# Kernel tuning notes

Measured on AMD Instinct MI355X. Metric: run time of the kernel, lower is better.

The kernel has to match this reference:

```python
import jax, jax.numpy as jnp
import numpy as np

B, T, E, H, D, NL = 2, 1024, 2048, 16, 128, 3
MAXL = T * (2 ** (NL - 1))  # k length doubles each layer: T, 2T, 4T


def _rms_norm(x, w, eps=1e-5):
    return x * jax.lax.rsqrt(jnp.mean(x * x, axis=-1, keepdims=True) + eps) * w


def _rope(x, cos, sin):
    # x: [B, S, H, D]; cos/sin: [>=S, D/2]; GPT-NeoX style (non-interleaved)
    S = x.shape[1]
    c = cos[:S][None, :, None, :]
    s = sin[:S][None, :, None, :]
    x1, x2 = jnp.split(x, 2, axis=-1)
    return jnp.concatenate([x1 * c - x2 * s, x1 * s + x2 * c], axis=-1)


def _causal_attn(q, k, v):
    # bottom-right-aligned causal (flash_attn_func causal=True with kv longer than q)
    Tq, L = q.shape[1], k.shape[1]
    scale = 1.0 / np.sqrt(q.shape[-1]).astype(np.float32)
    scores = jnp.einsum('bthd,bshd->bhts', q, k) * scale
    i = jnp.arange(Tq)[:, None]
    j = jnp.arange(L)[None, :]
    mask = j <= i + (L - Tq)
    scores = jnp.where(mask[None, None], scores, -jnp.inf)
    p = jax.nn.softmax(scores, axis=-1)
    return jnp.einsum('bhts,bshd->bthd', p, v)


def setup_inputs() -> dict:
    key = jax.random.key(0)
    ks = jax.random.split(key, 6)
    x = jax.random.normal(ks[0], (B, T, E), dtype=jnp.float32)
    inv_freq = 1.0 / (10000.0 ** (np.arange(0, D, 2, dtype=np.float32) / D))  # [D/2]
    ang = np.arange(MAXL, dtype=np.float32)[:, None] * inv_freq[None, :]      # [MAXL, D/2]
    cos = jnp.asarray(np.cos(ang), dtype=jnp.float32)
    sin = jnp.asarray(np.sin(ang), dtype=jnp.float32)
    wq = jax.random.normal(ks[1], (NL, E, E), dtype=jnp.float32) * 0.02
    wk = jax.random.normal(ks[2], (NL, E, E), dtype=jnp.float32) * 0.02
    wv = jax.random.normal(ks[3], (NL, E, E), dtype=jnp.float32) * 0.02
    ln_w = jnp.ones((NL, E), dtype=jnp.float32)
    lambdas = jnp.zeros((NL,), dtype=jnp.float32)
    w_out = jax.random.normal(ks[4], (E, E), dtype=jnp.float32) * 0.02
    final_ln_w = jnp.ones((E,), dtype=jnp.float32)
    alpha = jnp.ones((1,), dtype=jnp.float32)
    return {'x': x, 'cos': cos, 'sin': sin, 'wq': wq, 'wk': wk, 'wv': wv,
            'ln_w': ln_w, 'lambdas': lambdas, 'w_out': w_out,
            'final_ln_w': final_ln_w, 'alpha': alpha}


def reference(x, cos, sin, wq, wk, wv, ln_w, lambdas, w_out, final_ln_w, alpha):
    bsz, tgt_len, embed_dim = x.shape
    # lambda weights: sigmoid then LayerNorm over the NL scalars (no affine)
    lam = jax.nn.sigmoid(lambdas)
    lam = (lam - jnp.mean(lam)) * jax.lax.rsqrt(jnp.var(lam) + 1e-5)
    acc_k, acc_v = [], []
    total = jnp.zeros_like(x)
    for i in range(NL):  # small fixed layer count
        q = (x @ wq[i].T).reshape(bsz, tgt_len, H, D)
        k = (x @ wk[i].T).reshape(bsz, tgt_len, H, D)
        v = (x @ wv[i].T).reshape(bsz, tgt_len, H, D)
        if i > 0:
            k = jnp.concatenate([k] + acc_k, axis=1)
            v = jnp.concatenate([v] + acc_v, axis=1)
        q = _rope(q, cos, sin)
        k = _rope(k, cos, sin)  # note: cached K gets rotary re-applied, as in source
        attn = _causal_attn(q, k, v).reshape(bsz, tgt_len, embed_dim)
        attn = _rms_norm(attn, ln_w[i])
        total = total + attn * lam[i]
        acc_k.append(k)
        acc_v.append(v)
    out = _rms_norm(total + alpha * x, final_ln_w)
    return out @ w_out.T
```

## Files before the change

kernel.cpp:

```cpp
#include <hip/hip_runtime.h>
#include <hip/hip_bf16.h>

typedef unsigned short ushort_t;
typedef __attribute__((ext_vector_type(8))) short bf16x8;
typedef __attribute__((ext_vector_type(4))) short bf16x4;
typedef __attribute__((ext_vector_type(4))) float f32x4;
typedef __attribute__((ext_vector_type(4))) unsigned short u16x4;
typedef __attribute__((ext_vector_type(4))) unsigned int u32x4;

#define DEV __device__ __forceinline__

DEV ushort_t f2bf(float f) {
  __hip_bfloat16 h = __float2bfloat16(f);
  return __builtin_bit_cast(unsigned short, h);
}
DEV float bf2f(ushort_t b) {
  union { float f; unsigned int u; } a; a.u = ((unsigned int)b) << 16;
  return a.f;
}
DEV void gload_lds16(const void* g, void* l) {
  __builtin_amdgcn_global_load_lds((const __attribute__((address_space(1))) void*)g,
                                   (__attribute__((address_space(3))) void*)l, 16, 0, 0);
}
DEV unsigned ldsaddr(const void* l) {
  return (unsigned)(unsigned long long)(const __attribute__((address_space(3))) void*)l;
}
template <int OFF>
DEV bf16x4 tr16o(unsigned a) {
  bf16x4 d;
  asm volatile("ds_read_b64_tr_b16 %0, %1 offset:%c2" : "=v"(d) : "v"(a), "i"(OFF));
  return d;
}
template <int OFF>
DEV bf16x8 ldsb128o(unsigned a) {
  bf16x8 d;
  asm volatile("ds_read_b128 %0, %1 offset:%c2" : "=v"(d) : "v"(a), "i"(OFF));
  return d;
}

__global__ __launch_bounds__(256) void f2b_kernel(const float* __restrict__ in,
                                                  ushort_t* __restrict__ out, int n) {
  int base = (blockIdx.x * 256 + threadIdx.x) * 4;
  if (base >= n) return;
  f32x4 v = *(const f32x4*)(in + base);
  u16x4 o;
  o.x = f2bf(v.x); o.y = f2bf(v.y); o.z = f2bf(v.z); o.w = f2bf(v.w);
  *(u16x4*)(out + base) = o;
}

__global__ __launch_bounds__(256) void f2b3_kernel(const float* __restrict__ a, const float* __restrict__ b,
                                                   const float* __restrict__ c, ushort_t* __restrict__ out) {
  int id = blockIdx.x * 256 + threadIdx.x;
  int sel = id >> 20, k = (id & 1048575) * 4;
  const float* src = sel == 0 ? a : sel == 1 ? b : c;
  f32x4 v = *(const f32x4*)(src + k);
  u16x4 o;
  o.x = f2bf(v.x); o.y = f2bf(v.y); o.z = f2bf(v.z); o.w = f2bf(v.w);
  *(u16x4*)(out + (size_t)sel * 4194304 + k) = o;
}

__global__ void lam_kernel(const float* __restrict__ lambdas, float* __restrict__ lam) {
  if (threadIdx.x == 0 && blockIdx.x == 0) {
    float l0 = 1.f / (1.f + __expf(-lambdas[0]));
    float l1 = 1.f / (1.f + __expf(-lambdas[1]));
    float l2 = 1.f / (1.f + __expf(-lambdas[2]));
    float mean = (l0 + l1 + l2) * (1.f / 3.f);
    float d0 = l0 - mean, d1 = l1 - mean, d2 = l2 - mean;
    float var = (d0 * d0 + d1 * d1 + d2 * d2) * (1.f / 3.f);
    float rs = rsqrtf(var + 1e-5f);
    lam[0] = d0 * rs; lam[1] = d1 * rs; lam[2] = d2 * rs;
  }
}

DEV void gemm_core(const ushort_t* __restrict__ A, const ushort_t* __restrict__ Bm,
                   ushort_t* lsA, ushort_t* lsB, int bm, int bn, int kbeg, int kend,
                   f32x4 (&acc)[4][4]) {
  const int K = 2048;
  int tid = threadIdx.x;
  int w = tid >> 6, lane = tid & 63;
  int g = lane >> 4, r = lane & 15;
  int wm = w >> 1, wn = w & 1;
#pragma unroll
  for (int i = 0; i < 4; ++i)
#pragma unroll
    for (int j = 0; j < 4; ++j) acc[i][j] = 0.f;

  for (int kk = kbeg; kk < kend; kk += 32) {
    __syncthreads();
#pragma unroll
    for (int j2 = 0; j2 < 2; ++j2) {
      int eb = w * 1024 + j2 * 512;
      int ebl = eb + lane * 8;
      int rr = ebl >> 5, cc = ebl & 31;
      gload_lds16(A + (size_t)(bm * 128 + rr) * K + kk + cc, lsA + eb);
      gload_lds16(Bm + (size_t)(bn * 128 + rr) * K + kk + cc, lsB + eb);
    }
    __syncthreads();
    bf16x8 af[4], bfr[4];
#pragma unroll
    for (int i = 0; i < 4; ++i)
      af[i] = *(const bf16x8*)(lsA + (wm * 64 + i * 16 + r) * 32 + g * 8);
#pragma unroll
    for (int j = 0; j < 4; ++j)
      bfr[j] = *(const bf16x8*)(lsB + (wn * 64 + j * 16 + r) * 32 + g * 8);
#pragma unroll
    for (int i = 0; i < 4; ++i)
#pragma unroll
      for (int j = 0; j < 4; ++j)
        acc[i][j] = __builtin_amdgcn_mfma_f32_16x16x32_bf16(af[i], bfr[j], acc[i][j], 0, 0, 0);
  }
}

__global__ __launch_bounds__(256) void gemm_qkv(
    const ushort_t* __restrict__ A,
    const ushort_t* __restrict__ Bq, const ushort_t* __restrict__ Bk, const ushort_t* __restrict__ Bv,
    ushort_t* __restrict__ Cq, ushort_t* __restrict__ Ck, ushort_t* __restrict__ Cv, int Lkv) {
  __shared__ __align__(16) ushort_t lsA[4096];
  __shared__ __align__(16) ushort_t lsB[4096];
  int sel = blockIdx.x >> 4, bn = blockIdx.x & 15, bm = blockIdx.y;
  const ushort_t* Bm = (sel == 0) ? Bq : (sel == 1) ? Bk : Bv;
  ushort_t* C = (sel == 0) ? Cq : (sel == 1) ? Ck : Cv;
  int Lsel = (sel == 0) ? 1024 : Lkv;
  f32x4 acc[4][4];
  gemm_core(A, Bm, lsA, lsB, bm, bn, 0, 2048, acc);
  int lane = threadIdx.x & 63, w = threadIdx.x >> 6;
  int g = lane >> 4, r = lane & 15, wm = w >> 1, wn = w & 1;
#pragma unroll
  for (int i = 0; i < 4; ++i)
#pragma unroll
    for (int j = 0; j < 4; ++j) {
      int row0 = bm * 128 + wm * 64 + i * 16 + g * 4;
      int col = bn * 128 + wn * 64 + j * 16 + r;
#pragma unroll
      for (int t = 0; t < 4; ++t) {
        int row = row0 + t;
        int b2 = row >> 10, t2 = row & 1023;
        C[(size_t)(b2 * Lsel + t2) * 2048 + col] = f2bf(acc[i][j][t]);
      }
    }
}

__global__ __launch_bounds__(256) void gemm_bt_part(
    const ushort_t* __restrict__ A, const ushort_t* __restrict__ Bm, float* __restrict__ P) {
  __shared__ __align__(16) ushort_t lsA[4096];
  __shared__ __align__(16) ushort_t lsB[4096];
  int bn = blockIdx.x, bm = blockIdx.y, s = blockIdx.z;
  f32x4 acc[4][4];
  gemm_core(A, Bm, lsA, lsB, bm, bn, s * 1024, (s + 1) * 1024, acc);
  float* C = P + (size_t)s * 4194304;
  int lane = threadIdx.x & 63, w = threadIdx.x >> 6;
  int g = lane >> 4, r = lane & 15, wm = w >> 1, wn = w & 1;
#pragma unroll
  for (int i = 0; i < 4; ++i)
#pragma unroll
    for (int j = 0; j < 4; ++j) {
      int row0 = bm * 128 + wm * 64 + i * 16 + g * 4;
      int col = bn * 128 + wn * 64 + j * 16 + r;
#pragma unroll
      for (int t = 0; t < 4; ++t)
        C[(size_t)(row0 + t) * 2048 + col] = acc[i][j][t];
    }
}

__global__ __launch_bounds__(256) void add2_kernel(const float* __restrict__ a, const float* __restrict__ b,
                                                   float* __restrict__ out) {
  int i = (blockIdx.x * 256 + threadIdx.x) * 4;
  f32x4 va = *(const f32x4*)(a + i);
  f32x4 vb = *(const f32x4*)(b + i);
  f32x4 r;
#pragma unroll
  for (int k = 0; k < 4; ++k) r[k] = va[k] + vb[k];
  *(f32x4*)(out + i) = r;
}

DEV void rope_body(const ushort_t* src, ushort_t* dst, const float* cosT, const float* sinT,
                   int Ls, int s0, int Ld, int dpos0, int cnt, int bp) {
  int b = bp / cnt, pidx = bp % cnt;
  int pos = dpos0 + pidx;
  int pi = threadIdx.x * 4;
  int h = pi >> 6, d = pi & 63;
  const ushort_t* s_ = src + ((size_t)(b * Ls + s0 + pidx) * 16 + h) * 128 + d;
  ushort_t* d_ = dst + ((size_t)(b * Ld + pos) * 16 + h) * 128 + d;
  f32x4 c4 = *(const f32x4*)(cosT + (size_t)pos * 64 + d);
  f32x4 s4 = *(const f32x4*)(sinT + (size_t)pos * 64 + d);
  u16x4 x1 = *(const u16x4*)(s_);
  u16x4 x2 = *(const u16x4*)(s_ + 64);
  u16x4 o1, o2;
#pragma unroll
  for (int k = 0; k < 4; ++k) {
    float a = bf2f(x1[k]), bb = bf2f(x2[k]);
    o1[k] = f2bf(a * c4[k] - bb * s4[k]);
    o2[k] = f2bf(a * s4[k] + bb * c4[k]);
  }
  *(u16x4*)d_ = o1;
  *(u16x4*)(d_ + 64) = o2;
}
DEV void copy_body(const ushort_t* src, ushort_t* dst, int Ls, int s0, int Ld, int dpos0,
                   int cnt, int bp) {
  int b = bp / cnt, pidx = bp % cnt;
  const u32x4* s = (const u32x4*)(src + (size_t)(b * Ls + s0 + pidx) * 2048);
  u32x4* d = (u32x4*)(dst + (size_t)(b * Ld + dpos0 + pidx) * 2048);
  d[threadIdx.x] = s[threadIdx.x];
}

__global__ __launch_bounds__(256) void rope_k(ushort_t* Kc, const float* __restrict__ cosT,
                                              const float* __restrict__ sinT, int L) {
  rope_body(Kc, Kc, cosT, sinT, L, 0, L, 0, 1024, blockIdx.x);
}

__global__ __launch_bounds__(256) void layer1_cache(const ushort_t* __restrict__ K0, ushort_t* __restrict__ K1,
                                                    const ushort_t* __restrict__ V0, ushort_t* __restrict__ V1,
                                                    const float* __restrict__ cosT, const float* __restrict__ sinT) {
  int bp = blockIdx.x;
  if (bp < 2048) rope_body(K0, K1, cosT, sinT, 1024, 0, 2048, 1024, 1024, bp);
  else copy_body(V0, V1, 1024, 0, 2048, 1024, 1024, bp - 2048);
}

__global__ __launch_bounds__(256) void layer2_cache(const ushort_t* __restrict__ K1, ushort_t* __restrict__ K2,
                                                    const ushort_t* __restrict__ V1, ushort_t* __restrict__ V2,
                                                    const float* __restrict__ cosT, const float* __restrict__ sinT) {
  int bp = blockIdx.x;
  if (bp < 2048) copy_body(K1, K2, 2048, 1024, 4096, 1024, 1024, bp);
  else if (bp < 6144) rope_body(K1, K2, cosT, sinT, 2048, 0, 4096, 2048, 2048, bp - 2048);
  else if (bp < 8192) copy_body(V1, V2, 2048, 1024, 4096, 1024, 1024, bp - 6144);
  else copy_body(V1, V2, 2048, 0, 4096, 2048, 2048, bp - 8192);
}

__global__ __launch_bounds__(256, 4) void attn_kernel(
    const ushort_t* __restrict__ Qraw, const ushort_t* __restrict__ Kc, const ushort_t* __restrict__ Vc,
    const float* __restrict__ cosT, const float* __restrict__ sinT,
    ushort_t* __restrict__ Opart, float2* __restrict__ Ml, int Lk) {
  __shared__ __align__(16) ushort_t lsK[8192];
  __shared__ __align__(16) ushort_t lsV[8192];
  const float SC2 = 0.1275174366f;

  int bid = (int)blockIdx.x;
  int swz = (bid & 7) * 128 + (bid >> 3);
  int s = swz & 1;
  int rest = swz >> 1;

  int w = threadIdx.x >> 6, lane = threadIdx.x & 63;
  int bq = rest & 15, h = (rest >> 4) & 15, b = rest >> 8;
  int qt = bq * 4 + w;
  int g = lane >> 4, r = lane & 15;
  int off = Lk - 1024;

  const ushort_t* qbase = Qraw + ((size_t)(b * 1024 + qt * 16 + r) * 16 + h) * 128;
  int pos = qt * 16 + r;
  const float* cb = cosT + (size_t)pos * 64;
  const float* sb = sinT + (size_t)pos * 64;
  bf16x8 qf[4];
#pragma unroll
  for (int c = 0; c < 2; ++c) {
    int d0 = c * 32 + g * 8;
    f32x4 c0 = *(const f32x4*)(cb + d0);
    f32x4 c1 = *(const f32x4*)(cb + d0 + 4);
    f32x4 s0 = *(const f32x4*)(sb + d0);
    f32x4 s1 = *(const f32x4*)(sb + d0 + 4);
    bf16x8 x1 = *(const bf16x8*)(qbase + d0);
    bf16x8 x2 = *(const bf16x8*)(qbase + d0 + 64);
    bf16x8 lo, hi;
#pragma unroll
    for (int k = 0; k < 8; ++k) {
      float cv = (k < 4 ? c0[k] : c1[k - 4]) * SC2;
      float sv = (k < 4 ? s0[k] : s1[k - 4]) * SC2;
      float a = bf2f((ushort_t)x1[k]);
      float bb = bf2f((ushort_t)x2[k]);
      lo[k] = (short)f2bf(a * cv - bb * sv);
      hi[k] = (short)f2bf(a * sv + bb * cv);
    }
    qf[c] = lo; qf[c + 2] = hi;
  }

  int t = threadIdx.x;
  int krow0 = t >> 4,        kc0 = (t & 15) ^ (krow0 & 7);
  int krow1 = (t + 256) >> 4, kc1 = (t & 15) ^ (krow1 & 7);
  const size_t adv = 32 * 2048;
  const size_t adv2 = 2 * adv;
  const ushort_t* srcK0 = Kc + ((size_t)(b * Lk + krow0) * 16 + h) * 128 + kc0 * 8 + s * adv;
  const ushort_t* srcK1 = Kc + ((size_t)(b * Lk + krow1) * 16 + h) * 128 + kc1 * 8 + s * adv;
  int L0 = t, L1 = t + 256;
  int vrow0 = ((L0 >> 3) & 7) * 4 + ((L0 >> 1) & 3), vd0 = (L0 >> 6) * 16 + (L0 & 1) * 8;
  int vrow1 = ((L1 >> 3) & 7) * 4 + ((L1 >> 1) & 3), vd1 = (L1 >> 6) * 16 + (L1 & 1) * 8;
  const ushort_t* srcV0 = Vc + ((size_t)(b * Lk + vrow0) * 16 + h) * 128 + vd0 + s * adv;
  const ushort_t* srcV1 = Vc + ((size_t)(b * Lk + vrow1) * 16 + h) * 128 + vd1 + s * adv;

  auto STAGE = [&](int buf) {
    ushort_t* k0 = lsK + buf * 4096 + w * 512;
    ushort_t* v0 = lsV + buf * 4096 + w * 512;
    gload_lds16(srcK0, k0);
    gload_lds16(srcK1, k0 + 2048);
    gload_lds16(srcV0, v0);
    gload_lds16(srcV1, v0 + 2048);
    srcK0 += adv2; srcK1 += adv2; srcV0 += adv2; srcV1 += adv2;
  };

  unsigned kx[4];
  unsigned kbase0 = ldsaddr(lsK) + (unsigned)(r * 256);
#pragma unroll
  for (int c = 0; c < 4; ++c)
    kx[c] = kbase0 + (unsigned)((((c * 32 + g * 8) ^ ((r & 7) * 8))) * 2);
  unsigned vbase0 = ldsaddr(lsV);

  float m_run = -1e30f, l_run = 0.f;
  f32x4 o[8];
#pragma unroll
  for (int c = 0; c < 8; ++c) o[c] = 0.f;

  int qp = qt * 16 + r + off;
  int qmin = qt * 16 + off;
  int nkt_w = ((qt * 16 + 15 + off) >> 5) + 1;
  int nkt_blk = (((bq * 4 + 3) * 16 + 15 + off) >> 5) + 1;
  int ntile = (nkt_blk - s + 1) >> 1;

#define LDK(c, ks) ldsb128o<(ks) * 4096>(kx[c] + kb)
#define LDV(hh, i) tr16o<(hh) * 4096 + (i) * 512>(vb)

  if (ntile > 0) {
    STAGE(0);
    for (int it = 0; it < ntile; ++it) {
      int kt = s + it * 2;
      int cur = it & 1;
      if (it + 1 < ntile) {
        STAGE(cur ^ 1);
        asm volatile("s_waitcnt vmcnt(4)" ::: "memory");
      } else {
        asm volatile("s_waitcnt vmcnt(0)" ::: "memory");
      }
      __builtin_amdgcn_s_barrier();
      __builtin_amdgcn_sched_barrier(0);
      if (kt < nkt_w) {
        unsigned kb = (unsigned)(cur << 13);
        unsigned vb = vbase0 + kb;
        f32x4 st[2];
        {
          bf16x8 k0 = LDK(0, 0), k1 = LDK(1, 0), k2 = LDK(2, 0), k3 = LDK(3, 0);
          asm volatile("s_waitcnt lgkmcnt(0)" ::: "memory");
          __builtin_amdgcn_sched_barrier(0);
          __builtin_amdgcn_s_setprio(1);
          f32x4 acc = 0.f;
          acc = __builtin_amdgcn_mfma_f32_16x16x32_bf16(k0, qf[0], acc, 0, 0, 0);
          acc = __builtin_amdgcn_mfma_f32_16x16x32_bf16(k1, qf[1], acc, 0, 0, 0);
          acc = __builtin_amdgcn_mfma_f32_16x16x32_bf16(k2, qf[2], acc, 0, 0, 0);
          acc = __builtin_amdgcn_mfma_f32_16x16x32_bf16(k3, qf[3], acc, 0, 0, 0);
          __builtin_amdgcn_s_setprio(0);
          st[0] = acc;
        }
        {
          bf16x8 k0 = LDK(0, 1), k1 = LDK(1, 1), k2 = LDK(2, 1), k3 = LDK(3, 1);
          asm volatile("s_waitcnt lgkmcnt(0)" ::: "memory");
          __builtin_amdgcn_sched_barrier(0);
          __builtin_amdgcn_s_setprio(1);
          f32x4 acc = 0.f;
          acc = __builtin_amdgcn_mfma_f32_16x16x32_bf16(k0, qf[0], acc, 0, 0, 0);
          acc = __builtin_amdgcn_mfma_f32_16x16x32_bf16(k1, qf[1], acc, 0, 0, 0);
          acc = __builtin_amdgcn_mfma_f32_16x16x32_bf16(k2, qf[2], acc, 0, 0, 0);
          acc = __builtin_amdgcn_mfma_f32_16x16x32_bf16(k3, qf[3], acc, 0, 0, 0);
          __builtin_amdgcn_s_setprio(0);
          st[1] = acc;
        }
        float pmax = -1e30f;
        int kp0 = kt * 32;
        if (kp0 + 31 > qmin) {
#pragma unroll
          for (int ks = 0; ks < 2; ++ks)
#pragma unroll
            for (int j = 0; j < 4; ++j) {
              int key = kp0 + ks * 16 + g * 4 + j;
              float sv = st[ks][j];
              if (key > qp) sv = -1e30f;
              st[ks][j] = sv;
              pmax = fmaxf(pmax, sv);
            }
        } else {
#pragma unroll
          for (int ks = 0; ks < 2; ++ks)
#pragma unroll
            for (int j = 0; j < 4; ++j) pmax = fmaxf(pmax, st[ks][j]);
        }
        pmax = fmaxf(pmax, __shfl_xor(pmax, 16, 64));
        pmax = fmaxf(pmax, __shfl_xor(pmax, 32, 64));
        if (!__all(pmax <= m_run + 11.5f)) {
          float mnew = fmaxf(m_run, pmax);
          float corr = exp2f(m_run - mnew);
          l_run *= corr;
#pragma unroll
          for (int c = 0; c < 8; ++c)
#pragma unroll
            for (int tt = 0; tt < 4; ++tt) o[c][tt] *= corr;
          m_run = mnew;
        }
        float psum = 0.f;
        bf16x4 pf[2];
#pragma unroll
        for (int ks = 0; ks < 2; ++ks)
#pragma unroll
          for (int j = 0; j < 4; ++j) {
            float pe = exp2f(st[ks][j] - m_run);
            psum += pe;
            pf[ks][j] = (short)f2bf(pe);
          }
        psum += __shfl_xor(psum, 16, 64);
        psum += __shfl_xor(psum, 32, 64);
        l_run += psum;
        {
          bf16x4 v0 = LDV(0, 0), v1 = LDV(0, 1), v2 = LDV(0, 2), v3 = LDV(0, 3);
          bf16x4 v4 = LDV(0, 4), v5 = LDV(0, 5), v6 = LDV(0, 6), v7 = LDV(0, 7);
          asm volatile("s_waitcnt lgkmcnt(0)" ::: "memory");
          __builtin_amdgcn_sched_barrier(0);
          __builtin_amdgcn_s_setprio(1);
          o[0] = __builtin_amdgcn_mfma_f32_16x16x16bf16_1k(v0, pf[0], o[0], 0, 0, 0);
          o[0] = __builtin_amdgcn_mfma_f32_16x16x16bf16_1k(v1, pf[1], o[0], 0, 0, 0);
          o[1] = __builtin_amdgcn_mfma_f32_16x16x16bf16_1k(v2, pf[0], o[1], 0, 0, 0);
          o[1] = __builtin_amdgcn_mfma_f32_16x16x16bf16_1k(v3, pf[1], o[1], 0, 0, 0);
          o[2] = __builtin_amdgcn_mfma_f32_16x16x16bf16_1k(v4, pf[0], o[2], 0, 0, 0);
          o[2] = __builtin_amdgcn_mfma_f32_16x16x16bf16_1k(v5, pf[1], o[2], 0, 0, 0);
          o[3] = __builtin_amdgcn_mfma_f32_16x16x16bf16_1k(v6, pf[0], o[3], 0, 0, 0);
          o[3] = __builtin_amdgcn_mfma_f32_16x16x16bf16_1k(v7, pf[1], o[3], 0, 0, 0);
          __builtin_amdgcn_s_setprio(0);
        }
        {
          bf16x4 v0 = LDV(1, 0), v1 = LDV(1, 1), v2 = LDV(1, 2), v3 = LDV(1, 3);
          bf16x4 v4 = LDV(1, 4), v5 = LDV(1, 5), v6 = LDV(1, 6), v7 = LDV(1, 7);
          asm volatile("s_waitcnt lgkmcnt(0)" ::: "memory");
          __builtin_amdgcn_sched_barrier(0);
          __builtin_amdgcn_s_setprio(1);
          o[4] = __builtin_amdgcn_mfma_f32_16x16x16bf16_1k(v0, pf[0], o[4], 0, 0, 0);
          o[4] = __builtin_amdgcn_mfma_f32_16x16x16bf16_1k(v1, pf[1], o[4], 0, 0, 0);
          o[5] = __builtin_amdgcn_mfma_f32_16x16x16bf16_1k(v2, pf[0], o[5], 0, 0, 0);
          o[5] = __builtin_amdgcn_mfma_f32_16x16x16bf16_1k(v3, pf[1], o[5], 0, 0, 0);
          o[6] = __builtin_amdgcn_mfma_f32_16x16x16bf16_1k(v4, pf[0], o[6], 0, 0, 0);
          o[6] = __builtin_amdgcn_mfma_f32_16x16x16bf16_1k(v5, pf[1], o[6], 0, 0, 0);
          o[7] = __builtin_amdgcn_mfma_f32_16x16x16bf16_1k(v6, pf[0], o[7], 0, 0, 0);
          o[7] = __builtin_amdgcn_mfma_f32_16x16x16bf16_1k(v7, pf[1], o[7], 0, 0, 0);
          __builtin_amdgcn_s_setprio(0);
        }
      }
      __builtin_amdgcn_sched_barrier(0);
      __builtin_amdgcn_s_barrier();
    }
  }
#undef LDK
#undef LDV
  ushort_t* ob = Opart + (size_t)s * 4194304 + ((size_t)(b * 1024 + qt * 16 + r) * 16 + h) * 128;
#pragma unroll
  for (int dblk = 0; dblk < 8; ++dblk) {
    u16x4 ov;
#pragma unroll
    for (int tt = 0; tt < 4; ++tt) ov[tt] = f2bf(o[dblk][tt]);
    *(u16x4*)(ob + dblk * 16 + g * 4) = ov;
  }
  if (g == 0) {
    float2 ml; ml.x = m_run; ml.y = l_run;
    Ml[((size_t)(s * 2 + b) * 1024 + qt * 16 + r) * 16 + h] = ml;
  }
}

template <int FIRST>
__global__ __launch_bounds__(256) void rms_combine(const ushort_t* __restrict__ Opart, const float2* __restrict__ Ml,
                                                   const float* __restrict__ lnw, const float* __restrict__ lam,
                                                   int li, float* __restrict__ total) {
  int row = blockIdx.x;
  int t8 = threadIdx.x * 8;
  int h = t8 >> 7;
  float2 ml0 = Ml[(size_t)row * 16 + h];
  float2 ml1 = Ml[(size_t)(row + 2048) * 16 + h];
  float M = fmaxf(ml0.x, ml1.x);
  float w0 = exp2f(ml0.x - M), w1 = exp2f(ml1.x - M);
  float rinv = 1.f / (w0 * ml0.y + w1 * ml1.y);
  w0 *= rinv; w1 *= rinv;
  const ushort_t* a0 = Opart + (size_t)row * 2048 + t8;
  const ushort_t* a1 = a0 + 4194304;
  u16x4 p00 = *(const u16x4*)(a0);
  u16x4 p01 = *(const u16x4*)(a0 + 4);
  u16x4 p10 = *(const u16x4*)(a1);
  u16x4 p11 = *(const u16x4*)(a1 + 4);
  f32x4 v0, v1;
#pragma unroll
  for (int k = 0; k < 4; ++k) {
    v0[k] = w0 * bf2f(p00[k]) + w1 * bf2f(p10[k]);
    v1[k] = w0 * bf2f(p01[k]) + w1 * bf2f(p11[k]);
  }
  float ss = v0.x * v0.x + v0.y * v0.y + v0.z * v0.z + v0.w * v0.w +
             v1.x * v1.x + v1.y * v1.y + v1.z * v1.z + v1.w * v1.w;
#pragma unroll
  for (int m = 1; m < 64; m <<= 1) ss += __shfl_xor(ss, m, 64);
  __shared__ float red[4];
  int w = threadIdx.x >> 6, lane = threadIdx.x & 63;
  if (lane == 0) red[w] = ss;
  __syncthreads();
  ss = red[0] + red[1] + red[2] + red[3];
  float sca = rsqrtf(ss * (1.f / 2048.f) + 1e-5f) * lam[li];
  f32x4 w0v = *(const f32x4*)(lnw + t8);
  f32x4 w1v = *(const f32x4*)(lnw + t8 + 4);
  float* o = total + (size_t)row * 2048 + t8;
  f32x4 r0, r1;
#pragma unroll
  for (int k = 0; k < 4; ++k) { r0[k] = v0[k] * sca * w0v[k]; r1[k] = v1[k] * sca * w1v[k]; }
  if (!FIRST) {
    f32x4 q0 = *(const f32x4*)(o);
    f32x4 q1 = *(const f32x4*)(o + 4);
#pragma unroll
    for (int k = 0; k < 4; ++k) { r0[k] += q0[k]; r1[k] += q1[k]; }
  }
  *(f32x4*)(o) = r0;
  *(f32x4*)(o + 4) = r1;
}

__global__ __launch_bounds__(256) void final_norm(const float* __restrict__ total, const float* __restrict__ x,
                                                  const float* __restrict__ alphap, const float* __restrict__ flw,
                                                  ushort_t* __restrict__ ybf) {
  int row = blockIdx.x;
  float al = alphap[0];
  int t8 = threadIdx.x * 8;
  const float* tp = total + (size_t)row * 2048 + t8;
  const float* xp = x + (size_t)row * 2048 + t8;
  f32x4 t0 = *(const f32x4*)(tp);
  f32x4 t1 = *(const f32x4*)(tp + 4);
  f32x4 x0 = *(const f32x4*)(xp);
  f32x4 x1 = *(const f32x4*)(xp + 4);
  float y[8];
#pragma unroll
  for (int k = 0; k < 4; ++k) { y[k] = t0[k] + al * x0[k]; y[4 + k] = t1[k] + al * x1[k]; }
  float ss = 0.f;
#pragma unroll
  for (int k = 0; k < 8; ++k) ss += y[k] * y[k];
#pragma unroll
  for (int m = 1; m < 64; m <<= 1) ss += __shfl_xor(ss, m, 64);
  __shared__ float red[4];
  int w = threadIdx.x >> 6, lane = threadIdx.x & 63;
  if (lane == 0) red[w] = ss;
  __syncthreads();
  ss = red[0] + red[1] + red[2] + red[3];
  float s = rsqrtf(ss * (1.f / 2048.f) + 1e-5f);
  f32x4 w0 = *(const f32x4*)(flw + t8);
  f32x4 w1 = *(const f32x4*)(flw + t8 + 4);
  u16x4 o0, o1;
#pragma unroll
  for (int k = 0; k < 4; ++k) {
    o0[k] = f2bf(y[k] * s * w0[k]);
    o1[k] = f2bf(y[4 + k] * s * w1[k]);
  }
  *(u16x4*)(ybf + (size_t)row * 2048 + t8) = o0;
  *(u16x4*)(ybf + (size_t)row * 2048 + t8 + 4) = o1;
}

extern "C" void kernel_launch(void* const* d_in, const int* in_sizes, int n_in,
                              void* d_out, int out_size, void* d_ws, size_t ws_size,
                              hipStream_t stream) {
  const float* x = (const float*)d_in[0];
  const float* cosT = (const float*)d_in[1];
  const float* sinT = (const float*)d_in[2];
  const float* wq = (const float*)d_in[3];
  const float* wk = (const float*)d_in[4];
  const float* wv = (const float*)d_in[5];
  const float* lnw = (const float*)d_in[6];
  const float* lambdas = (const float*)d_in[7];
  const float* w_out = (const float*)d_in[8];
  const float* flw = (const float*)d_in[9];
  const float* alpha = (const float*)d_in[10];

  const size_t ME = 4194304ull;
  char* p = (char*)d_ws;
  size_t off = 0;
  auto alc = [&](size_t bytes) -> void* {
    void* r = p + off;
    off += (bytes + 255) & ~(size_t)255;
    return r;
  };
  ushort_t* xb = (ushort_t*)alc(ME * 2);
  void* uni = alc(2 * ME * 4);
  ushort_t* wl = (ushort_t*)uni;
  ushort_t* Opart = (ushort_t*)uni;
  float* Ppart = (float*)uni;
  ushort_t* q = (ushort_t*)alc(ME * 2);
  ushort_t* K0 = (ushort_t*)alc(ME * 2);
  ushort_t* K1 = (ushort_t*)alc(2 * ME * 2);
  ushort_t* K2 = (ushort_t*)alc(4 * ME * 2);
  ushort_t* V0 = (ushort_t*)alc(ME * 2);
  ushort_t* V1 = (ushort_t*)alc(2 * ME * 2);
  ushort_t* V2 = (ushort_t*)alc(4 * ME * 2);
  float* total = (float*)alc(ME * 4);
  float2* Ml = (float2*)alc(65536 * 8);
  float* lam = (float*)alc(256);
  ushort_t* ybf = q;
  ushort_t* wob = K0;

  f2b_kernel<<<4096, 256, 0, stream>>>(x, xb, 4194304);
  lam_kernel<<<1, 64, 0, stream>>>(lambdas, lam);

  ushort_t* Kc[3] = {K0, K1, K2};
  ushort_t* Vc[3] = {V0, V1, V2};

  for (int li = 0; li < 3; ++li) {
    int L = 1024 << li;
    size_t woff = (size_t)li * ME;
    f2b3_kernel<<<12288, 256, 0, stream>>>(wq + woff, wk + woff, wv + woff, wl);
    gemm_qkv<<<dim3(48, 16), 256, 0, stream>>>(xb, wl, wl + ME, wl + 2 * ME,
                                               q, Kc[li], Vc[li], L);
    rope_k<<<2048, 256, 0, stream>>>(Kc[li], cosT, sinT, L);
    if (li == 1)
      layer1_cache<<<4096, 256, 0, stream>>>(K0, K1, V0, V1, cosT, sinT);
    else if (li == 2)
      layer2_cache<<<12288, 256, 0, stream>>>(K1, K2, V1, V2, cosT, sinT);
    attn_kernel<<<1024, 256, 0, stream>>>(q, Kc[li], Vc[li], cosT, sinT, Opart, Ml, L);
    if (li == 0)
      rms_combine<1><<<2048, 256, 0, stream>>>(Opart, Ml, lnw, lam, 0, total);
    else
      rms_combine<0><<<2048, 256, 0, stream>>>(Opart, Ml, lnw + (size_t)li * 2048, lam, li, total);
  }

  f2b_kernel<<<4096, 256, 0, stream>>>(w_out, wob, 4194304);
  final_norm<<<2048, 256, 0, stream>>>(total, x, alpha, flw, ybf);
  gemm_bt_part<<<dim3(16, 16, 2), 256, 0, stream>>>(ybf, wob, Ppart);
  add2_kernel<<<4096, 256, 0, stream>>>(Ppart, Ppart + ME, (float*)d_out);
}
```

Baseline: 560.8 us.

## Replace QKV GEMM with 256x256-tile double-buffered MFMA kernel

Replaces the 128x128-tile QKV projection GEMM with a 512-thread, 256x256-tile kernel. It uses double-buffered LDS loaded directly from global memory, XOR-swizzled LDS addressing, and block-index swizzling. The main loop interleaves half-tile prefetches with four MFMA phases under explicit barriers, waitcnts and setprio. The aim is more reuse per loaded byte and global-load latency hidden behind compute. The cost is 128KB of LDS and only 192 blocks, which may underfill the CUs, plus fragile hand-tuned synchronisation.

```diff
diff --git a/kernel.cpp b/kernel.cpp
--- a/kernel.cpp
+++ b/kernel.cpp
@@ -111,34 +111,145 @@
   }
 }
 
-__global__ __launch_bounds__(256) void gemm_qkv(
+#define MM(i, j)                                                                              \
+  acc[i][j] = __builtin_amdgcn_mfma_f32_16x16x32_bf16(af[(i) & 3][0], bfr[j][0], acc[i][j], 0, 0, 0); \
+  acc[i][j] = __builtin_amdgcn_mfma_f32_16x16x32_bf16(af[(i) & 3][1], bfr[j][1], acc[i][j], 0, 0, 0);
+
+__global__ __launch_bounds__(512, 2) void gemm_qkv256(
     const ushort_t* __restrict__ A,
     const ushort_t* __restrict__ Bq, const ushort_t* __restrict__ Bk, const ushort_t* __restrict__ Bv,
     ushort_t* __restrict__ Cq, ushort_t* __restrict__ Ck, ushort_t* __restrict__ Cv, int Lkv) {
-  __shared__ __align__(16) ushort_t lsA[4096];
-  __shared__ __align__(16) ushort_t lsB[4096];
-  int sel = blockIdx.x >> 4, bn = blockIdx.x & 15, bm = blockIdx.y;
-  const ushort_t* Bm = (sel == 0) ? Bq : (sel == 1) ? Bk : Bv;
+  __shared__ __align__(16) ushort_t lsA[32768];
+  __shared__ __align__(16) ushort_t lsB[32768];
+  const int NT = 32;
+
+  int bid = (int)blockIdx.x;
+  int swz = (bid & 7) * 24 + (bid >> 3);
+  int bm = swz / 24;
+  int rest = swz % 24;
+  int sel = rest >> 3, bnc = rest & 7;
+  const ushort_t* Bmat = (sel == 0) ? Bq : (sel == 1) ? Bk : Bv;
   ushort_t* C = (sel == 0) ? Cq : (sel == 1) ? Ck : Cv;
   int Lsel = (sel == 0) ? 1024 : Lkv;
-  f32x4 acc[4][4];
-  gemm_core(A, Bm, lsA, lsB, bm, bn, 0, 2048, acc);
-  int lane = threadIdx.x & 63, w = threadIdx.x >> 6;
-  int g = lane >> 4, r = lane & 15, wm = w >> 1, wn = w & 1;
-#pragma unroll
-  for (int i = 0; i < 4; ++i)
+
+  int tid = threadIdx.x;
+  int wv = tid >> 6, lane = tid & 63;
+  int wm = wv >> 2, wn = wv & 3;
+  int g = lane >> 4, r = lane & 15;
+
+  int row0 = tid >> 3, c0 = tid & 7;
+  int colsw = (c0 ^ (row0 & 7)) * 8;
+  const ushort_t* pA0 = A + (size_t)(bm * 256 + row0) * 2048 + colsw;
+  const ushort_t* pB0 = Bmat + (size_t)(bnc * 256 + row0) * 2048 + colsw;
+  ushort_t* dA = lsA + tid * 8;
+  ushort_t* dB = lsB + tid * 8;
+
+  auto SA = [&](int T, int hh) {
+    const ushort_t* s = pA0 + (size_t)(hh * 128) * 2048 + (size_t)T * 64;
+    ushort_t* d = dA + (T & 1) * 16384 + hh * 8192;
+    gload_lds16(s, d);
+    gload_lds16(s + (size_t)64 * 2048, d + 4096);
+  };
+  auto SB = [&](int T, int hh) {
+    const ushort_t* s = pB0 + (size_t)(hh * 128) * 2048 + (size_t)T * 64;
+    ushort_t* d = dB + (T & 1) * 16384 + hh * 8192;
+    gload_lds16(s, d);
+    gload_lds16(s + (size_t)64 * 2048, d + 4096);
+  };
+
+  unsigned xm = (unsigned)(r & 7);
+  unsigned aAb = ldsaddr(lsA) + (unsigned)((wm * 128 + r) * 128);
+  unsigned aA0b = aAb + ((((unsigned)g) ^ xm) << 4);
+  unsigned aA1b = aAb + ((((unsigned)(4 + g)) ^ xm) << 4);
+  unsigned aBb = ldsaddr(lsB) + (unsigned)((wn * 64 + r) * 128);
+  unsigned aB0b = aBb + ((((unsigned)g) ^ xm) << 4);
+  unsigned aB1b = aBb + ((((unsigned)(4 + g)) ^ xm) << 4);
+
+  f32x4 acc[8][4];
+#pragma unroll
+  for (int i = 0; i < 8; ++i)
+#pragma unroll
+    for (int j = 0; j < 4; ++j) acc[i][j] = 0.f;
+  bf16x8 af[4][2], bfr[4][2];
+
+  SA(0, 0); SB(0, 0); SB(0, 1); SA(0, 1);
+  SA(1, 0); SB(1, 0); SB(1, 1);
+  asm volatile("s_waitcnt vmcnt(6)" ::: "memory");
+  __builtin_amdgcn_s_barrier();
+  __builtin_amdgcn_sched_barrier(0);
+
+  for (int t = 0; t < NT; ++t) {
+    unsigned cb = (unsigned)((t & 1) << 15);
+    unsigned A0 = aA0b + cb, A1 = aA1b + cb, B0 = aB0b + cb, B1 = aB1b + cb;
+    bool full = (t < NT - 2);
+    af[0][0] = ldsb128o<0>(A0);     af[0][1] = ldsb128o<0>(A1);
+    af[1][0] = ldsb128o<2048>(A0);  af[1][1] = ldsb128o<2048>(A1);
+    af[2][0] = ldsb128o<4096>(A0);  af[2][1] = ldsb128o<4096>(A1);
+    af[3][0] = ldsb128o<6144>(A0);  af[3][1] = ldsb128o<6144>(A1);
+    bfr[0][0] = ldsb128o<0>(B0);    bfr[0][1] = ldsb128o<0>(B1);
+    bfr[1][0] = ldsb128o<2048>(B0); bfr[1][1] = ldsb128o<2048>(B1);
+    if (t + 1 < NT) SA(t + 1, 1);
+    __builtin_amdgcn_s_barrier();
+    asm volatile("s_waitcnt lgkmcnt(0)" ::: "memory");
+    __builtin_amdgcn_sched_barrier(0);
+    __builtin_amdgcn_s_setprio(1);
+    MM(0, 0) MM(1, 0) MM(2, 0) MM(3, 0) MM(0, 1) MM(1, 1) MM(2, 1) MM(3, 1)
+    __builtin_amdgcn_s_setprio(0);
+    __builtin_amdgcn_sched_barrier(0);
+    __builtin_amdgcn_s_barrier();
+    bfr[2][0] = ldsb128o<4096>(B0); bfr[2][1] = ldsb128o<4096>(B1);
+    bfr[3][0] = ldsb128o<6144>(B0); bfr[3][1] = ldsb128o<6144>(B1);
+    if (full) SA(t + 2, 0);
+    __builtin_amdgcn_s_barrier();
+    asm volatile("s_waitcnt lgkmcnt(0)" ::: "memory");
+    __builtin_amdgcn_sched_barrier(0);
+    __builtin_amdgcn_s_setprio(1);
+    MM(0, 2) MM(1, 2) MM(2, 2) MM(3, 2) MM(0, 3) MM(1, 3) MM(2, 3) MM(3, 3)
+    __builtin_amdgcn_s_setprio(0);
+    if (full) { asm volatile("s_waitcnt vmcnt(4)" ::: "memory"); }
+    else      { asm volatile("s_waitcnt vmcnt(0)" ::: "memory"); }
+    __builtin_amdgcn_sched_barrier(0);
+    __builtin_amdgcn_s_barrier();
+    af[0][0] = ldsb128o<8192>(A0);  af[0][1] = ldsb128o<8192>(A1);
+    af[1][0] = ldsb128o<10240>(A0); af[1][1] = ldsb128o<10240>(A1);
+    af[2][0] = ldsb128o<12288>(A0); af[2][1] = ldsb128o<12288>(A1);
+    af[3][0] = ldsb128o<14336>(A0); af[3][1] = ldsb128o<14336>(A1);
+    if (full) SB(t + 2, 0);
+    __builtin_amdgcn_s_barrier();
+    asm volatile("s_waitcnt lgkmcnt(0)" ::: "memory");
+    __builtin_amdgcn_sched_barrier(0);
+    __builtin_amdgcn_s_setprio(1);
+    MM(4, 2) MM(5, 2) MM(6, 2) MM(7, 2) MM(4, 3) MM(5, 3) MM(6, 3) MM(7, 3)
+    __builtin_amdgcn_s_setprio(0);
+    __builtin_amdgcn_sched_barrier(0);
+    __builtin_amdgcn_s_barrier();
+    if (full) SB(t + 2, 1);
+    __builtin_amdgcn_s_barrier();
+    __builtin_amdgcn_s_setprio(1);
+    MM(4, 0) MM(5, 0) MM(6, 0) MM(7, 0) MM(4, 1) MM(5, 1) MM(6, 1) MM(7, 1)
+    __builtin_amdgcn_s_setprio(0);
+    if (full) { asm volatile("s_waitcnt vmcnt(8)" ::: "memory"); }
+    else      { asm volatile("s_waitcnt vmcnt(0)" ::: "memory"); }
+    __builtin_amdgcn_sched_barrier(0);
+    __builtin_amdgcn_s_barrier();
+  }
+
+  int prow = bm * 256 + wm * 128 + g * 4;
+  int pcol = bnc * 256 + wn * 64 + r;
+#pragma unroll
+  for (int i = 0; i < 8; ++i)
 #pragma unroll
     for (int j = 0; j < 4; ++j) {
-      int row0 = bm * 128 + wm * 64 + i * 16 + g * 4;
-      int col = bn * 128 + wn * 64 + j * 16 + r;
-#pragma unroll
-      for (int t = 0; t < 4; ++t) {
-        int row = row0 + t;
+      int col = pcol + j * 16;
+#pragma unroll
+      for (int tt = 0; tt < 4; ++tt) {
+        int row = prow + i * 16 + tt;
         int b2 = row >> 10, t2 = row & 1023;
-        C[(size_t)(b2 * Lsel + t2) * 2048 + col] = f2bf(acc[i][j][t]);
+        C[(size_t)(b2 * Lsel + t2) * 2048 + col] = f2bf(acc[i][j][tt]);
       }
     }
 }
+#undef MM
 
 __global__ __launch_bounds__(256) void gemm_bt_part(
     const ushort_t* __restrict__ A, const ushort_t* __restrict__ Bm, float* __restrict__ P) {
@@ -596,8 +707,8 @@
     int L = 1024 << li;
     size_t woff = (size_t)li * ME;
     f2b3_kernel<<<12288, 256, 0, stream>>>(wq + woff, wk + woff, wv + woff, wl);
-    gemm_qkv<<<dim3(48, 16), 256, 0, stream>>>(xb, wl, wl + ME, wl + 2 * ME,
-                                               q, Kc[li], Vc[li], L);
+    gemm_qkv256<<<192, 512, 0, stream>>>(xb, wl, wl + ME, wl + 2 * ME,
+                                         q, Kc[li], Vc[li], L);
     rope_k<<<2048, 256, 0, stream>>>(Kc[li], cosT, sinT, L);
     if (li == 1)
       layer1_cache<<<4096, 256, 0, stream>>>(K0, K1, V0, V1, cosT, sinT);
```

Result: faster. 543.1 us (-3.1%).
